# Performance work log

Measured on AMD Instinct MI355X. Metric: run time of the kernel, lower is better.

## Reference

```python
import jax, jax.numpy as jnp
import numpy as np

N_USERS, N_MOVIES = 200000, 80000
E, L = 2000000, 500000
D, H = 128, 64


def _mean_agg(x_src, src, dst, n_dst):
    # gather source features along edges and mean-reduce per destination node
    msg = x_src[src]                                        # [E, F]
    s = jax.ops.segment_sum(msg, dst, num_segments=n_dst)   # [n_dst, F]
    c = jax.ops.segment_sum(jnp.ones(src.shape, x_src.dtype), dst, num_segments=n_dst)
    return s / jnp.maximum(c, 1.0)[:, None]


def _sage(x_src, x_dst, src, dst, n_dst, Wl, b, Wr):
    # PyG SAGEConv (mean aggr): lin_l(mean_j x_j) + lin_r(x_dst); lin_r has no bias
    return _mean_agg(x_src, src, dst, n_dst) @ Wl + b + x_dst @ Wr


def setup_inputs() -> dict:
    key = jax.random.key(0)
    ks = jax.random.split(key, 24)
    inp = {
        "x_user": jax.random.normal(ks[0], (N_USERS, D), jnp.float32),
        "x_movie": jax.random.normal(ks[1], (N_MOVIES, D), jnp.float32),
        "edge_src": jax.random.randint(ks[2], (E,), 0, N_USERS, jnp.int32),
        "edge_dst": jax.random.randint(ks[3], (E,), 0, N_MOVIES, jnp.int32),
        "lbl_src": jax.random.randint(ks[4], (L,), 0, N_USERS, jnp.int32),
        "lbl_dst": jax.random.randint(ks[5], (L,), 0, N_MOVIES, jnp.int32),
    }
    def w(k, shape):
        fan_in = shape[0]
        return jax.random.uniform(k, shape, jnp.float32, -1.0, 1.0) / np.sqrt(fan_in)
    # layer 1 (src_dim D -> H), one SAGEConv per relation
    inp["W1_u2m_l"] = w(ks[6], (D, H)); inp["b1_u2m"] = jnp.zeros((H,), jnp.float32)
    inp["W1_u2m_r"] = w(ks[7], (D, H))
    inp["W1_m2u_l"] = w(ks[8], (D, H)); inp["b1_m2u"] = jnp.zeros((H,), jnp.float32)
    inp["W1_m2u_r"] = w(ks[9], (D, H))
    # layer 2 (H -> H)
    inp["W2_u2m_l"] = w(ks[10], (H, H)); inp["b2_u2m"] = jnp.zeros((H,), jnp.float32)
    inp["W2_u2m_r"] = w(ks[11], (H, H))
    inp["W2_m2u_l"] = w(ks[12], (H, H)); inp["b2_m2u"] = jnp.zeros((H,), jnp.float32)
    inp["W2_m2u_r"] = w(ks[13], (H, H))
    # edge decoder MLP
    inp["Wd1"] = w(ks[14], (2 * H, H)); inp["bd1"] = jnp.zeros((H,), jnp.float32)
    inp["Wd2"] = w(ks[15], (H, 1)); inp["bd2"] = jnp.zeros((1,), jnp.float32)
    return inp


def reference(x_user, x_movie, edge_src, edge_dst, lbl_src, lbl_dst,
              W1_u2m_l, b1_u2m, W1_u2m_r, W1_m2u_l, b1_m2u, W1_m2u_r,
              W2_u2m_l, b2_u2m, W2_u2m_r, W2_m2u_l, b2_m2u, W2_m2u_r,
              Wd1, bd1, Wd2, bd2):
    # hetero layer 1 (user->movie and movie->user reverse relation), then ReLU
    h_m = jax.nn.relu(_sage(x_user, x_movie, edge_src, edge_dst, N_MOVIES,
                            W1_u2m_l, b1_u2m, W1_u2m_r))
    h_u = jax.nn.relu(_sage(x_movie, x_user, edge_dst, edge_src, N_USERS,
                            W1_m2u_l, b1_m2u, W1_m2u_r))
    # hetero layer 2 (no activation, matching GNNEncoder)
    z_m = _sage(h_u, h_m, edge_src, edge_dst, N_MOVIES, W2_u2m_l, b2_u2m, W2_u2m_r)
    z_u = _sage(h_m, h_u, edge_dst, edge_src, N_USERS, W2_m2u_l, b2_m2u, W2_m2u_r)
    # edge decoder: gather-concat-MLP
    z = jnp.concatenate([z_u[lbl_src], z_m[lbl_dst]], axis=-1)  # [L, 2H]
    z = jax.nn.relu(z @ Wd1 + bd1)
    return (z @ Wd2 + bd2).reshape(-1)
```

## Files before the change

### kernel.cpp

```cpp
#include <hip/hip_runtime.h>
#include <stdint.h>

#define BW   128
#define NBM  625
#define NBU  1563
#define CAPM 4096
#define CAPU 2048

typedef __attribute__((ext_vector_type(8))) short bf16x8;
typedef __attribute__((ext_vector_type(4))) float f32x4;

__device__ __forceinline__ float b2f(ushort u) {
    return __uint_as_float((uint32_t)u << 16);
}
__device__ __forceinline__ ushort f2b(float f) {
    uint32_t x = __float_as_uint(f);
    return (ushort)((x + 0x7FFFu + ((x >> 16) & 1u)) >> 16);
}
__device__ __forceinline__ float lo16f(uint32_t v) { return __uint_as_float(v << 16); }
__device__ __forceinline__ float hi16f(uint32_t v) { return __uint_as_float(v & 0xFFFF0000u); }
__device__ __forceinline__ uint32_t packbf2(float x, float y) {
    return (uint32_t)f2b(x) | ((uint32_t)f2b(y) << 16);
}

__global__ __launch_bounds__(256) void bin_kernel(
    const int* __restrict__ src, const int* __restrict__ dst, int E,
    int* __restrict__ gcm, int* __restrict__ gcu,
    uint32_t* __restrict__ Bm, uint32_t* __restrict__ Bu)
{
    __shared__ int hm[NBM], hu[NBU];
    const int CH = 8192;
    int e0 = blockIdx.x * CH;
    int e1 = min(e0 + CH, E);
    int tid = threadIdx.x;
    for (int b = tid; b < NBM; b += 256) hm[b] = 0;
    for (int b = tid; b < NBU; b += 256) hu[b] = 0;
    __syncthreads();
    for (int i = e0 + tid; i < e1; i += 256) {
        atomicAdd(&hm[dst[i] >> 7], 1);
        atomicAdd(&hu[src[i] >> 7], 1);
    }
    __syncthreads();
    for (int b = tid; b < NBM; b += 256) { int c = hm[b]; hm[b] = c ? atomicAdd(&gcm[b], c) : 0; }
    for (int b = tid; b < NBU; b += 256) { int c = hu[b]; hu[b] = c ? atomicAdd(&gcu[b], c) : 0; }
    __syncthreads();
    for (int i = e0 + tid; i < e1; i += 256) {
        int d = dst[i], s = src[i];
        int bm = d >> 7, bu = s >> 7;
        int pm = atomicAdd(&hm[bm], 1);
        if (pm < CAPM) Bm[(size_t)bm * CAPM + pm] = ((uint32_t)(d & 127) << 24) | (uint32_t)s;
        int pu = atomicAdd(&hu[bu], 1);
        if (pu < CAPU) Bu[(size_t)bu * CAPU + pu] = ((uint32_t)(s & 127) << 24) | (uint32_t)d;
    }
}

__global__ __launch_bounds__(256) void sort_bucket2(
    uint32_t* __restrict__ Bm, const int* __restrict__ gcm, int* __restrict__ loffm,
    uint32_t* __restrict__ Bu, const int* __restrict__ gcu, int* __restrict__ loffu)
{
    __shared__ uint32_t rec[CAPM];
    __shared__ uint32_t srt[CAPM];
    __shared__ int hist[BW];
    __shared__ int hoff[BW + 1];
    __shared__ int cur[BW];
    int bid = blockIdx.x, tid = threadIdx.x;
    uint32_t* B; const int* gc; int* loff; int cap; int b;
    if (bid < NBM) { B = Bm; gc = gcm; loff = loffm; cap = CAPM; b = bid; }
    else           { B = Bu; gc = gcu; loff = loffu; cap = CAPU; b = bid - NBM; }
    int cnt = min(gc[b], cap);
    uint32_t* bp = B + (size_t)b * cap;
    for (int i = tid; i < cnt; i += 256) rec[i] = bp[i];
    if (tid < BW) hist[tid] = 0;
    __syncthreads();
    for (int i = tid; i < cnt; i += 256) atomicAdd(&hist[rec[i] >> 24], 1);
    __syncthreads();
    if (tid == 0) {
        int s = 0;
        for (int i = 0; i < BW; ++i) { hoff[i] = s; s += hist[i]; }
        hoff[BW] = s;
    }
    __syncthreads();
    if (tid < BW) cur[tid] = hoff[tid];
    __syncthreads();
    for (int i = tid; i < cnt; i += 256) {
        uint32_t r = rec[i];
        int pos = atomicAdd(&cur[r >> 24], 1);
        srt[pos] = (r & 0xFFFFFFu) << 5;
    }
    __syncthreads();
    for (int i = tid; i < cnt; i += 256) bp[i] = srt[i];
    for (int i = tid; i <= BW; i += 256) loff[(size_t)b * (BW + 1) + i] = hoff[i];
}

__global__ __launch_bounds__(256) void wprep(
    const float* __restrict__ W2ml, const float* __restrict__ W2mr,
    const float* __restrict__ W2ul, const float* __restrict__ W2ur,
    const float* __restrict__ Wd1, const float* __restrict__ bd1,
    const float* __restrict__ b2m, const float* __restrict__ b2u,
    const float* __restrict__ W1ul, const float* __restrict__ W1mr,
    const float* __restrict__ W1ml, const float* __restrict__ W1ur,
    ushort* __restrict__ Wt2_m, ushort* __restrict__ Wt2_u,
    ushort* __restrict__ Wt_u, ushort* __restrict__ Wt_m,
    float* __restrict__ cu, float* __restrict__ cm)
{
    __shared__ float As[4096], Bs[4096];
    int bid = blockIdx.x, tid = threadIdx.x;
    if (bid < 4) {
        const float* A; int brow0; const float* bvec; const float* addb;
        ushort* WtOut; int cofs; float* outc;
        if (bid == 0)      { A = W2ml; brow0 = 0;  bvec = b2m; addb = bd1;    WtOut = Wt2_m; cofs = 0;  outc = cu; }
        else if (bid == 1) { A = W2mr; brow0 = 0;  bvec = 0;   addb = 0;      WtOut = Wt2_u; cofs = 0;  outc = 0;  }
        else if (bid == 2) { A = W2ul; brow0 = 64; bvec = b2u; addb = 0;      WtOut = Wt2_u; cofs = 64; outc = cm; }
        else               { A = W2ur; brow0 = 64; bvec = 0;   addb = 0;      WtOut = Wt2_m; cofs = 64; outc = 0;  }
        for (int i = tid; i < 4096; i += 256) {
            As[i] = A[i];
            Bs[i] = Wd1[(size_t)(brow0 + (i >> 6)) * 64 + (i & 63)];
        }
        __syncthreads();
        int r = tid >> 2, c0 = (tid & 3) * 16;
        float acc[16] = {};
        for (int k = 0; k < 64; ++k) {
            float a = As[r * 64 + k];
            const float* bp = &Bs[k * 64 + c0];
#pragma unroll
            for (int j = 0; j < 16; ++j) acc[j] += a * bp[j];
        }
#pragma unroll
        for (int j = 0; j < 16; ++j)
            WtOut[(size_t)(cofs + c0 + j) * 64 + r] = f2b(acc[j]);
        if (outc && tid < 64) {
            float s = addb ? addb[tid] : 0.f;
            for (int k = 0; k < 64; ++k) s += bvec[k] * Bs[k * 64 + tid];
            outc[tid] = s;
        }
    } else {
        int t = bid - 4;
        const float *Wa, *Wb; ushort* Wt;
        if (t < 64) { Wa = W1ul; Wb = W1mr; Wt = Wt_u; }
        else        { Wa = W1ml; Wb = W1ur; Wt = Wt_m; t -= 64; }
        int idx = t * 256 + tid;
        int c = idx >> 7, k = idx & 127;
        Wt[idx] = f2b((c < 64 ? Wa : Wb)[(size_t)k * 64 + (c & 63)]);
    }
}

template<int RELU>
__global__ __launch_bounds__(256) void agg_csr(
    const uint32_t* __restrict__ Ba, const int* __restrict__ loffa, int capa,
    const uint32_t* __restrict__ ta, const uint32_t* __restrict__ sa,
    const float* __restrict__ biasa, uint32_t* __restrict__ oa, int na, int GA,
    const uint32_t* __restrict__ Bb, const int* __restrict__ loffb, int capb,
    const uint32_t* __restrict__ tb, const uint32_t* __restrict__ sb,
    const float* __restrict__ biasb, uint32_t* __restrict__ ob, int nb)
{
    int bid = blockIdx.x;
    const uint32_t* B; const int* loff; int cap;
    const uint32_t* table; const uint32_t* self; const float* bias;
    uint32_t* out; int n_nodes; int lb;
    if (bid < GA) { B = Ba; loff = loffa; cap = capa; table = ta; self = sa; bias = biasa; out = oa; n_nodes = na; lb = bid; }
    else          { B = Bb; loff = loffb; cap = capb; table = tb; self = sb; bias = biasb; out = ob; n_nodes = nb; lb = bid - GA; }
    int node = lb * 4 + (threadIdx.x >> 6);
    if (node >= n_nodes) return;
    int lane = threadIdx.x & 63;
    int eq = lane >> 4;
    int fq = lane & 15;
    int b = node >> 7, l = node & 127;
    const int* lo = loff + (size_t)b * (BW + 1);
    int beg = lo[l], end = lo[l + 1];
    const uint32_t* bp = B + (size_t)b * cap;
    float a0 = 0.f, a1 = 0.f, a2 = 0.f, a3 = 0.f;
    int p = beg;
    for (; p + 32 <= end; p += 32) {
        uint32_t r0 = bp[p + eq];
        uint32_t r1 = bp[p + 4 + eq];
        uint32_t r2 = bp[p + 8 + eq];
        uint32_t r3 = bp[p + 12 + eq];
        uint32_t r4 = bp[p + 16 + eq];
        uint32_t r5 = bp[p + 20 + eq];
        uint32_t r6 = bp[p + 24 + eq];
        uint32_t r7 = bp[p + 28 + eq];
        uint2 v0 = *(const uint2*)&table[r0 + fq * 2];
        uint2 v1 = *(const uint2*)&table[r1 + fq * 2];
        uint2 v2 = *(const uint2*)&table[r2 + fq * 2];
        uint2 v3 = *(const uint2*)&table[r3 + fq * 2];
        uint2 v4 = *(const uint2*)&table[r4 + fq * 2];
        uint2 v5 = *(const uint2*)&table[r5 + fq * 2];
        uint2 v6 = *(const uint2*)&table[r6 + fq * 2];
        uint2 v7 = *(const uint2*)&table[r7 + fq * 2];
        a0 += lo16f(v0.x) + lo16f(v1.x) + lo16f(v2.x) + lo16f(v3.x)
            + lo16f(v4.x) + lo16f(v5.x) + lo16f(v6.x) + lo16f(v7.x);
        a1 += hi16f(v0.x) + hi16f(v1.x) + hi16f(v2.x) + hi16f(v3.x)
            + hi16f(v4.x) + hi16f(v5.x) + hi16f(v6.x) + hi16f(v7.x);
        a2 += lo16f(v0.y) + lo16f(v1.y) + lo16f(v2.y) + lo16f(v3.y)
            + lo16f(v4.y) + lo16f(v5.y) + lo16f(v6.y) + lo16f(v7.y);
        a3 += hi16f(v0.y) + hi16f(v1.y) + hi16f(v2.y) + hi16f(v3.y)
            + hi16f(v4.y) + hi16f(v5.y) + hi16f(v6.y) + hi16f(v7.y);
    }
    for (; p + 8 <= end; p += 8) {
        uint32_t r0 = bp[p + eq];
        uint32_t r1 = bp[p + 4 + eq];
        uint2 v0 = *(const uint2*)&table[r0 + fq * 2];
        uint2 v1 = *(const uint2*)&table[r1 + fq * 2];
        a0 += lo16f(v0.x) + lo16f(v1.x);
        a1 += hi16f(v0.x) + hi16f(v1.x);
        a2 += lo16f(v0.y) + lo16f(v1.y);
        a3 += hi16f(v0.y) + hi16f(v1.y);
    }
    if (p + 4 <= end) {
        uint32_t r = bp[p + eq];
        uint2 v = *(const uint2*)&table[r + fq * 2];
        a0 += lo16f(v.x); a1 += hi16f(v.x); a2 += lo16f(v.y); a3 += hi16f(v.y);
        p += 4;
    }
    if (eq < end - p) {
        uint32_t r = bp[p + eq];
        uint2 v = *(const uint2*)&table[r + fq * 2];
        a0 += lo16f(v.x); a1 += hi16f(v.x); a2 += lo16f(v.y); a3 += hi16f(v.y);
    }
    a0 += __shfl_xor(a0, 16, 64); a0 += __shfl_xor(a0, 32, 64);
    a1 += __shfl_xor(a1, 16, 64); a1 += __shfl_xor(a1, 32, 64);
    a2 += __shfl_xor(a2, 16, 64); a2 += __shfl_xor(a2, 32, 64);
    a3 += __shfl_xor(a3, 16, 64); a3 += __shfl_xor(a3, 32, 64);
    if (lane < 16) {
        int deg = end - beg;
        float inv = 1.f / (float)(deg > 0 ? deg : 1);
        uint2 sv = *(const uint2*)&self[(size_t)node * 32 + fq * 2];
        float4 bv = *(const float4*)&bias[fq * 4];
        float v0 = a0 * inv + bv.x + lo16f(sv.x);
        float v1 = a1 * inv + bv.y + hi16f(sv.x);
        float v2 = a2 * inv + bv.z + lo16f(sv.y);
        float v3 = a3 * inv + bv.w + hi16f(sv.y);
        if (RELU) {
            v0 = fmaxf(v0, 0.f); v1 = fmaxf(v1, 0.f);
            v2 = fmaxf(v2, 0.f); v3 = fmaxf(v3, 0.f);
        }
        *(uint2*)&out[(size_t)node * 32 + fq * 2] = make_uint2(packbf2(v0, v1), packbf2(v2, v3));
    }
}

__global__ __launch_bounds__(256) void gemm1_mfma(
    const float* __restrict__ Xu, const ushort* __restrict__ Wtu,
    ushort* __restrict__ Ua, ushort* __restrict__ Ub, int Mu, int GU,
    const float* __restrict__ Xm, const ushort* __restrict__ Wtm,
    ushort* __restrict__ Ma, ushort* __restrict__ Mb, int Mm)
{
    constexpr int K = 128;
    int bid = blockIdx.x;
    const float* X; const ushort* Wt; ushort *Ya, *Yb; int row0; int M;
    if (bid < GU) { X = Xu; Wt = Wtu; Ya = Ua; Yb = Ub; row0 = bid * 128; M = Mu; }
    else          { X = Xm; Wt = Wtm; Ya = Ma; Yb = Mb; row0 = (bid - GU) * 128; M = Mm; }
    int tid = threadIdx.x;
    int lane = tid & 63, wr = tid >> 6;
    int r0g = row0 + wr * 32 + (lane & 15);
    int r1g = r0g + 16;
    int kgrp = (lane >> 4) * 8;
    f32x4 acc0[8] = {}, acc1[8] = {};
#pragma unroll
    for (int ks = 0; ks < 4; ++ks) {
        int kb = kgrp + ks * 32;
        float4 z = make_float4(0.f, 0.f, 0.f, 0.f);
        float4 u0 = z, u1 = z, w0 = z, w1 = z;
        if (r0g < M) {
            u0 = *(const float4*)&X[(size_t)r0g * K + kb];
            u1 = *(const float4*)&X[(size_t)r0g * K + kb + 4];
        }
        if (r1g < M) {
            w0 = *(const float4*)&X[(size_t)r1g * K + kb];
            w1 = *(const float4*)&X[(size_t)r1g * K + kb + 4];
        }
        float xs0[8] = {u0.x, u0.y, u0.z, u0.w, u1.x, u1.y, u1.z, u1.w};
        float xs1[8] = {w0.x, w0.y, w0.z, w0.w, w1.x, w1.y, w1.z, w1.w};
        bf16x8 ah0, al0, ah1, al1;
#pragma unroll
        for (int j = 0; j < 8; ++j) {
            ushort h0 = f2b(xs0[j]);
            ah0[j] = (short)h0;
            al0[j] = (short)f2b(xs0[j] - b2f(h0));
            ushort h1 = f2b(xs1[j]);
            ah1[j] = (short)h1;
            al1[j] = (short)f2b(xs1[j] - b2f(h1));
        }
#pragma unroll
        for (int cb = 0; cb < 8; ++cb) {
            bf16x8 b = *(const bf16x8*)&Wt[(size_t)(cb * 16 + (lane & 15)) * K + kb];
            acc0[cb] = __builtin_amdgcn_mfma_f32_16x16x32_bf16(ah0, b, acc0[cb], 0, 0, 0);
            acc0[cb] = __builtin_amdgcn_mfma_f32_16x16x32_bf16(al0, b, acc0[cb], 0, 0, 0);
            acc1[cb] = __builtin_amdgcn_mfma_f32_16x16x32_bf16(ah1, b, acc1[cb], 0, 0, 0);
            acc1[cb] = __builtin_amdgcn_mfma_f32_16x16x32_bf16(al1, b, acc1[cb], 0, 0, 0);
        }
    }
#pragma unroll
    for (int cb = 0; cb < 8; ++cb) {
        ushort* Y = (cb < 4) ? Ya : Yb;
        int cc = (cb * 16 + (lane & 15)) & 63;
#pragma unroll
        for (int reg = 0; reg < 4; ++reg) {
            int g0 = row0 + wr * 32 + (lane >> 4) * 4 + reg;
            if (g0 < M) Y[(size_t)g0 * 64 + cc] = f2b(acc0[cb][reg]);
            int g1 = g0 + 16;
            if (g1 < M) Y[(size_t)g1 * 64 + cc] = f2b(acc1[cb][reg]);
        }
    }
}

__global__ __launch_bounds__(256) void gemm2_mfma(
    const ushort* __restrict__ Xu, const ushort* __restrict__ Wtu,
    ushort* __restrict__ Ua, ushort* __restrict__ Ub, int Mu, int GU,
    const ushort* __restrict__ Xm, const ushort* __restrict__ Wtm,
    ushort* __restrict__ Ma, ushort* __restrict__ Mb, int Mm)
{
    int bid = blockIdx.x;
    const ushort* X; const ushort* Wt; ushort *Ya, *Yb; int row0;
    if (bid < GU) { X = Xu; Wt = Wtu; Ya = Ua; Yb = Ub; row0 = bid * 64; }
    else          { X = Xm; Wt = Wtm; Ya = Ma; Yb = Mb; row0 = (bid - GU) * 64; }
    int tid = threadIdx.x;
    int lane = tid & 63, wr = tid >> 6;
    int rglob = row0 + wr * 16 + (lane & 15);
    int kgrp = (lane >> 4) * 8;
    f32x4 acc[8] = {};
#pragma unroll
    for (int ks = 0; ks < 2; ++ks) {
        bf16x8 a = *(const bf16x8*)&X[(size_t)rglob * 64 + kgrp + ks * 32];
#pragma unroll
        for (int cb = 0; cb < 8; ++cb) {
            bf16x8 b = *(const bf16x8*)&Wt[(size_t)(cb * 16 + (lane & 15)) * 64 + kgrp + ks * 32];
            acc[cb] = __builtin_amdgcn_mfma_f32_16x16x32_bf16(a, b, acc[cb], 0, 0, 0);
        }
    }
#pragma unroll
    for (int cb = 0; cb < 8; ++cb) {
        ushort* Y = (cb < 4) ? Ya : Yb;
        int cc = (cb * 16 + (lane & 15)) & 63;
#pragma unroll
        for (int reg = 0; reg < 4; ++reg) {
            int grow = row0 + wr * 16 + (lane >> 4) * 4 + reg;
            Y[(size_t)grow * 64 + cc] = f2b(acc[cb][reg]);
        }
    }
}

__global__ __launch_bounds__(256) void edge_dec(
    const uint32_t* __restrict__ Au, const uint32_t* __restrict__ Am,
    const int* __restrict__ ls, const int* __restrict__ ld,
    const float* __restrict__ Wd2, const float* __restrict__ bd2,
    float* __restrict__ out, int L)
{
    int e0 = blockIdx.x * 32 + (threadIdx.x >> 4) * 2;
    if (e0 >= L) return;
    int e1 = e0 + 1;
    bool has1 = (e1 < L);
    int fq = threadIdx.x & 15;
    float4 w = *(const float4*)&Wd2[fq * 4];
    uint2 a0 = *(const uint2*)&Au[(size_t)ls[e0] * 32 + fq * 2];
    uint2 m0 = *(const uint2*)&Am[(size_t)ld[e0] * 32 + fq * 2];
    uint2 a1 = make_uint2(0u, 0u), m1 = make_uint2(0u, 0u);
    if (has1) {
        a1 = *(const uint2*)&Au[(size_t)ls[e1] * 32 + fq * 2];
        m1 = *(const uint2*)&Am[(size_t)ld[e1] * 32 + fq * 2];
    }
    float v0 = fmaxf(lo16f(a0.x) + lo16f(m0.x), 0.f) * w.x
             + fmaxf(hi16f(a0.x) + hi16f(m0.x), 0.f) * w.y
             + fmaxf(lo16f(a0.y) + lo16f(m0.y), 0.f) * w.z
             + fmaxf(hi16f(a0.y) + hi16f(m0.y), 0.f) * w.w;
    float v1 = fmaxf(lo16f(a1.x) + lo16f(m1.x), 0.f) * w.x
             + fmaxf(hi16f(a1.x) + hi16f(m1.x), 0.f) * w.y
             + fmaxf(lo16f(a1.y) + lo16f(m1.y), 0.f) * w.z
             + fmaxf(hi16f(a1.y) + hi16f(m1.y), 0.f) * w.w;
#pragma unroll
    for (int msk = 8; msk >= 1; msk >>= 1) {
        v0 += __shfl_xor(v0, msk, 64);
        v1 += __shfl_xor(v1, msk, 64);
    }
    if (fq == 0) {
        float b = bd2[0];
        out[e0] = v0 + b;
        if (has1) out[e1] = v1 + b;
    }
}

extern "C" void kernel_launch(void* const* d_in, const int* in_sizes, int n_in,
                              void* d_out, int out_size, void* d_ws, size_t ws_size,
                              hipStream_t stream)
{
    const float* x_user  = (const float*)d_in[0];
    const float* x_movie = (const float*)d_in[1];
    const int*   esrc    = (const int*)d_in[2];
    const int*   edst    = (const int*)d_in[3];
    const int*   lsrc    = (const int*)d_in[4];
    const int*   ldst    = (const int*)d_in[5];
    const float* W1ul = (const float*)d_in[6];
    const float* b1u  = (const float*)d_in[7];
    const float* W1ur = (const float*)d_in[8];
    const float* W1ml = (const float*)d_in[9];
    const float* b1m  = (const float*)d_in[10];
    const float* W1mr = (const float*)d_in[11];
    const float* W2ul = (const float*)d_in[12];
    const float* b2u  = (const float*)d_in[13];
    const float* W2ur = (const float*)d_in[14];
    const float* W2ml = (const float*)d_in[15];
    const float* b2m  = (const float*)d_in[16];
    const float* W2mr = (const float*)d_in[17];
    const float* Wd1  = (const float*)d_in[18];
    const float* bd1  = (const float*)d_in[19];
    const float* Wd2  = (const float*)d_in[20];
    const float* bd2  = (const float*)d_in[21];
    float* out = (float*)d_out;

    const int NU = in_sizes[0] / 128;
    const int NM = in_sizes[1] / 128;
    const int E  = in_sizes[2];
    const int L  = in_sizes[4];

    char* ws = (char*)d_ws;
    const size_t SU = (size_t)NU * 64 * 2;
    const size_t SM = (size_t)NM * 64 * 2;
    ushort* U0 = (ushort*)(ws + 0);
    ushort* U1 = (ushort*)(ws + SU);
    ushort* U2 = (ushort*)(ws + 2 * SU);
    ushort* M0 = (ushort*)(ws + 3 * SU);
    ushort* M1 = (ushort*)(ws + 3 * SU + SM);
    ushort* M2 = (ushort*)(ws + 3 * SU + 2 * SM);
    size_t o = 3 * SU + 3 * SM;
    auto align256 = [](size_t x) { return (x + 255) & ~(size_t)255; };
    o = align256(o);
    int* gcm = (int*)(ws + o); o = align256(o + (size_t)(NBM + NBU) * 4);
    int* gcu = gcm + NBM;
    uint32_t* Bm = (uint32_t*)(ws + o); o = align256(o + (size_t)NBM * CAPM * 4);
    uint32_t* Bu = (uint32_t*)(ws + o); o = align256(o + (size_t)NBU * CAPU * 4);
    int* loffm = (int*)(ws + o); o = align256(o + (size_t)NBM * (BW + 1) * 4);
    int* loffu = (int*)(ws + o); o = align256(o + (size_t)NBU * (BW + 1) * 4);
    float* cu  = (float*)(ws + o); o = align256(o + 64 * 4);
    float* cm  = (float*)(ws + o); o = align256(o + 64 * 4);
    ushort* Wt_u  = (ushort*)(ws + o); o = align256(o + 128 * 128 * 2);
    ushort* Wt_m  = (ushort*)(ws + o); o = align256(o + 128 * 128 * 2);
    ushort* Wt2_m = (ushort*)(ws + o); o = align256(o + 128 * 64 * 2);
    ushort* Wt2_u = (ushort*)(ws + o); o = align256(o + 128 * 64 * 2);

    hipMemsetAsync(gcm, 0, (size_t)(NBM + NBU) * 4, stream);
    int nbins = (E + 8191) / 8192;
    bin_kernel<<<nbins, 256, 0, stream>>>(esrc, edst, E, gcm, gcu, Bm, Bu);
    sort_bucket2<<<NBM + NBU, 256, 0, stream>>>(Bm, gcm, loffm, Bu, gcu, loffu);

    wprep<<<4 + 128, 256, 0, stream>>>(W2ml, W2mr, W2ul, W2ur, Wd1, bd1, b2m, b2u,
                                       W1ul, W1mr, W1ml, W1ur,
                                       Wt2_m, Wt2_u, Wt_u, Wt_m, cu, cm);

    int g1u = (NU + 127) / 128, g1m = (NM + 127) / 128;
    int gu = NU / 64, gm = NM / 64;
    int agm = (NM + 3) / 4, agu = (NU + 3) / 4;

    gemm1_mfma<<<g1u + g1m, 256, 0, stream>>>(x_user, Wt_u, U0, U1, NU, g1u,
                                              x_movie, Wt_m, M0, M1, NM);

    agg_csr<1><<<agm + agu, 256, 0, stream>>>(
        Bm, loffm, CAPM, (const uint32_t*)U0, (const uint32_t*)M1, b1u, (uint32_t*)M2, NM, agm,
        Bu, loffu, CAPU, (const uint32_t*)M0, (const uint32_t*)U1, b1m, (uint32_t*)U2, NU);

    gemm2_mfma<<<gu + gm, 256, 0, stream>>>(U2, Wt2_u, U0, U1, NU, gu,
                                            M2, Wt2_m, M0, M1, NM);

    agg_csr<0><<<agm + agu, 256, 0, stream>>>(
        Bm, loffm, CAPM, (const uint32_t*)U1, (const uint32_t*)M1, cm, (uint32_t*)M2, NM, agm,
        Bu, loffu, CAPU, (const uint32_t*)M0, (const uint32_t*)U0, cu, (uint32_t*)U2, NU);

    int gl = (L + 31) / 32;
    edge_dec<<<gl, 256, 0, stream>>>((const uint32_t*)U2, (const uint32_t*)M2,
                                     lsrc, ldst, Wd2, bd2, out, L);
}
```

Baseline: 464.8 us.

## Merge binning with weight prep and bucket sort with first GEMM

```diff
diff --git a/kernel.cpp b/kernel.cpp
--- a/kernel.cpp
+++ b/kernel.cpp
@@ -23,50 +23,168 @@
     return (uint32_t)f2b(x) | ((uint32_t)f2b(y) << 16);
 }
 
-__global__ __launch_bounds__(256) void bin_kernel(
-    const int* __restrict__ src, const int* __restrict__ dst, int E,
+__global__ __launch_bounds__(256) void binprep(
+    const int* __restrict__ src, const int* __restrict__ dst, int E, int nbins,
     int* __restrict__ gcm, int* __restrict__ gcu,
-    uint32_t* __restrict__ Bm, uint32_t* __restrict__ Bu)
-{
-    __shared__ int hm[NBM], hu[NBU];
-    const int CH = 8192;
-    int e0 = blockIdx.x * CH;
-    int e1 = min(e0 + CH, E);
-    int tid = threadIdx.x;
-    for (int b = tid; b < NBM; b += 256) hm[b] = 0;
-    for (int b = tid; b < NBU; b += 256) hu[b] = 0;
-    __syncthreads();
-    for (int i = e0 + tid; i < e1; i += 256) {
-        atomicAdd(&hm[dst[i] >> 7], 1);
-        atomicAdd(&hu[src[i] >> 7], 1);
-    }
-    __syncthreads();
-    for (int b = tid; b < NBM; b += 256) { int c = hm[b]; hm[b] = c ? atomicAdd(&gcm[b], c) : 0; }
-    for (int b = tid; b < NBU; b += 256) { int c = hu[b]; hu[b] = c ? atomicAdd(&gcu[b], c) : 0; }
-    __syncthreads();
-    for (int i = e0 + tid; i < e1; i += 256) {
-        int d = dst[i], s = src[i];
-        int bm = d >> 7, bu = s >> 7;
-        int pm = atomicAdd(&hm[bm], 1);
-        if (pm < CAPM) Bm[(size_t)bm * CAPM + pm] = ((uint32_t)(d & 127) << 24) | (uint32_t)s;
-        int pu = atomicAdd(&hu[bu], 1);
-        if (pu < CAPU) Bu[(size_t)bu * CAPU + pu] = ((uint32_t)(s & 127) << 24) | (uint32_t)d;
-    }
-}
-
-__global__ __launch_bounds__(256) void sort_bucket2(
+    uint32_t* __restrict__ Bm, uint32_t* __restrict__ Bu,
+    const float* __restrict__ W2ml, const float* __restrict__ W2mr,
+    const float* __restrict__ W2ul, const float* __restrict__ W2ur,
+    const float* __restrict__ Wd1, const float* __restrict__ bd1,
+    const float* __restrict__ b2m, const float* __restrict__ b2u,
+    const float* __restrict__ W1ul, const float* __restrict__ W1mr,
+    const float* __restrict__ W1ml, const float* __restrict__ W1ur,
+    ushort* __restrict__ Wt2_m, ushort* __restrict__ Wt2_u,
+    ushort* __restrict__ Wt_u, ushort* __restrict__ Wt_m,
+    float* __restrict__ cu, float* __restrict__ cm)
+{
+    __shared__ float smem[8192];
+    int bid = blockIdx.x, tid = threadIdx.x;
+    if (bid < nbins) {
+        int* hm = (int*)smem;
+        int* hu = ((int*)smem) + NBM;
+        const int CH = 8192;
+        int e0 = bid * CH;
+        int e1 = min(e0 + CH, E);
+        for (int b = tid; b < NBM; b += 256) hm[b] = 0;
+        for (int b = tid; b < NBU; b += 256) hu[b] = 0;
+        __syncthreads();
+        for (int i = e0 + tid; i < e1; i += 256) {
+            atomicAdd(&hm[dst[i] >> 7], 1);
+            atomicAdd(&hu[src[i] >> 7], 1);
+        }
+        __syncthreads();
+        for (int b = tid; b < NBM; b += 256) { int c = hm[b]; hm[b] = c ? atomicAdd(&gcm[b], c) : 0; }
+        for (int b = tid; b < NBU; b += 256) { int c = hu[b]; hu[b] = c ? atomicAdd(&gcu[b], c) : 0; }
+        __syncthreads();
+        for (int i = e0 + tid; i < e1; i += 256) {
+            int d = dst[i], s = src[i];
+            int bm = d >> 7, bu = s >> 7;
+            int pm = atomicAdd(&hm[bm], 1);
+            if (pm < CAPM) Bm[(size_t)bm * CAPM + pm] = ((uint32_t)(d & 127) << 24) | (uint32_t)s;
+            int pu = atomicAdd(&hu[bu], 1);
+            if (pu < CAPU) Bu[(size_t)bu * CAPU + pu] = ((uint32_t)(s & 127) << 24) | (uint32_t)d;
+        }
+        return;
+    }
+    int wb = bid - nbins;
+    if (wb < 4) {
+        float* As = smem;
+        float* Bs = smem + 4096;
+        const float* A; int brow0; const float* bvec; const float* addb;
+        ushort* WtOut; int cofs; float* outc;
+        if (wb == 0)      { A = W2ml; brow0 = 0;  bvec = b2m; addb = bd1;    WtOut = Wt2_m; cofs = 0;  outc = cu; }
+        else if (wb == 1) { A = W2mr; brow0 = 0;  bvec = 0;   addb = 0;      WtOut = Wt2_u; cofs = 0;  outc = 0;  }
+        else if (wb == 2) { A = W2ul; brow0 = 64; bvec = b2u; addb = 0;      WtOut = Wt2_u; cofs = 64; outc = cm; }
+        else              { A = W2ur; brow0 = 64; bvec = 0;   addb = 0;      WtOut = Wt2_m; cofs = 64; outc = 0;  }
+        for (int i = tid; i < 4096; i += 256) {
+            As[i] = A[i];
+            Bs[i] = Wd1[(size_t)(brow0 + (i >> 6)) * 64 + (i & 63)];
+        }
+        __syncthreads();
+        int r = tid >> 2, c0 = (tid & 3) * 16;
+        float acc[16] = {};
+        for (int k = 0; k < 64; ++k) {
+            float a = As[r * 64 + k];
+            const float* bp = &Bs[k * 64 + c0];
+#pragma unroll
+            for (int j = 0; j < 16; ++j) acc[j] += a * bp[j];
+        }
+#pragma unroll
+        for (int j = 0; j < 16; ++j)
+            WtOut[(size_t)(cofs + c0 + j) * 64 + r] = f2b(acc[j]);
+        if (outc && tid < 64) {
+            float s = addb ? addb[tid] : 0.f;
+            for (int k = 0; k < 64; ++k) s += bvec[k] * Bs[k * 64 + tid];
+            outc[tid] = s;
+        }
+    } else {
+        int t = wb - 4;
+        const float *Wa, *Wb; ushort* Wt;
+        if (t < 64) { Wa = W1ul; Wb = W1mr; Wt = Wt_u; }
+        else        { Wa = W1ml; Wb = W1ur; Wt = Wt_m; t -= 64; }
+        int idx = t * 256 + tid;
+        int c = idx >> 7, k = idx & 127;
+        Wt[idx] = f2b((c < 64 ? Wa : Wb)[(size_t)k * 64 + (c & 63)]);
+    }
+}
+
+__global__ __launch_bounds__(256) void sortgemm1(
+    const float* __restrict__ Xu, const ushort* __restrict__ Wtu,
+    ushort* __restrict__ Ua, ushort* __restrict__ Ub, int Mu, int GU,
+    const float* __restrict__ Xm, const ushort* __restrict__ Wtm,
+    ushort* __restrict__ Ma, ushort* __restrict__ Mb, int Mm, int NG,
     uint32_t* __restrict__ Bm, const int* __restrict__ gcm, int* __restrict__ loffm,
     uint32_t* __restrict__ Bu, const int* __restrict__ gcu, int* __restrict__ loffu)
 {
-    __shared__ uint32_t rec[CAPM];
-    __shared__ uint32_t srt[CAPM];
-    __shared__ int hist[BW];
-    __shared__ int hoff[BW + 1];
-    __shared__ int cur[BW];
+    __shared__ uint32_t smem[2 * CAPM + 3 * BW + 1];
     int bid = blockIdx.x, tid = threadIdx.x;
+    if (bid < NG) {
+        constexpr int K = 128;
+        const float* X; const ushort* Wt; ushort *Ya, *Yb; int row0; int M;
+        if (bid < GU) { X = Xu; Wt = Wtu; Ya = Ua; Yb = Ub; row0 = bid * 128; M = Mu; }
+        else          { X = Xm; Wt = Wtm; Ya = Ma; Yb = Mb; row0 = (bid - GU) * 128; M = Mm; }
+        int lane = tid & 63, wr = tid >> 6;
+        int r0g = row0 + wr * 32 + (lane & 15);
+        int r1g = r0g + 16;
+        int kgrp = (lane >> 4) * 8;
+        f32x4 acc0[8] = {}, acc1[8] = {};
+#pragma unroll
+        for (int ks = 0; ks < 4; ++ks) {
+            int kb = kgrp + ks * 32;
+            float4 z = make_float4(0.f, 0.f, 0.f, 0.f);
+            float4 u0 = z, u1 = z, w0 = z, w1 = z;
+            if (r0g < M) {
+                u0 = *(const float4*)&X[(size_t)r0g * K + kb];
+                u1 = *(const float4*)&X[(size_t)r0g * K + kb + 4];
+            }
+            if (r1g < M) {
+                w0 = *(const float4*)&X[(size_t)r1g * K + kb];
+                w1 = *(const float4*)&X[(size_t)r1g * K + kb + 4];
+            }
+            float xs0[8] = {u0.x, u0.y, u0.z, u0.w, u1.x, u1.y, u1.z, u1.w};
+            float xs1[8] = {w0.x, w0.y, w0.z, w0.w, w1.x, w1.y, w1.z, w1.w};
+            bf16x8 ah0, al0, ah1, al1;
+#pragma unroll
+            for (int j = 0; j < 8; ++j) {
+                ushort h0 = f2b(xs0[j]);
+                ah0[j] = (short)h0;
+                al0[j] = (short)f2b(xs0[j] - b2f(h0));
+                ushort h1 = f2b(xs1[j]);
+                ah1[j] = (short)h1;
+                al1[j] = (short)f2b(xs1[j] - b2f(h1));
+            }
+#pragma unroll
+            for (int cb = 0; cb < 8; ++cb) {
+                bf16x8 b = *(const bf16x8*)&Wt[(size_t)(cb * 16 + (lane & 15)) * K + kb];
+                acc0[cb] = __builtin_amdgcn_mfma_f32_16x16x32_bf16(ah0, b, acc0[cb], 0, 0, 0);
+                acc0[cb] = __builtin_amdgcn_mfma_f32_16x16x32_bf16(al0, b, acc0[cb], 0, 0, 0);
+                acc1[cb] = __builtin_amdgcn_mfma_f32_16x16x32_bf16(ah1, b, acc1[cb], 0, 0, 0);
+                acc1[cb] = __builtin_amdgcn_mfma_f32_16x16x32_bf16(al1, b, acc1[cb], 0, 0, 0);
+            }
+        }
+#pragma unroll
+        for (int cb = 0; cb < 8; ++cb) {
+            ushort* Y = (cb < 4) ? Ya : Yb;
+            int cc = (cb * 16 + (lane & 15)) & 63;
+#pragma unroll
+            for (int reg = 0; reg < 4; ++reg) {
+                int g0 = row0 + wr * 32 + (lane >> 4) * 4 + reg;
+                if (g0 < M) Y[(size_t)g0 * 64 + cc] = f2b(acc0[cb][reg]);
+                int g1 = g0 + 16;
+                if (g1 < M) Y[(size_t)g1 * 64 + cc] = f2b(acc1[cb][reg]);
+            }
+        }
+        return;
+    }
+    int sbid = bid - NG;
+    uint32_t* rec = smem;
+    uint32_t* srt = smem + CAPM;
+    int* hist = (int*)(smem + 2 * CAPM);
+    int* hoff = hist + BW;
+    int* cur  = hoff + BW + 1;
     uint32_t* B; const int* gc; int* loff; int cap; int b;
-    if (bid < NBM) { B = Bm; gc = gcm; loff = loffm; cap = CAPM; b = bid; }
-    else           { B = Bu; gc = gcu; loff = loffu; cap = CAPU; b = bid - NBM; }
+    if (sbid < NBM) { B = Bm; gc = gcm; loff = loffm; cap = CAPM; b = sbid; }
+    else            { B = Bu; gc = gcu; loff = loffu; cap = CAPU; b = sbid - NBM; }
     int cnt = min(gc[b], cap);
     uint32_t* bp = B + (size_t)b * cap;
     for (int i = tid; i < cnt; i += 256) rec[i] = bp[i];
@@ -90,58 +208,6 @@
     __syncthreads();
     for (int i = tid; i < cnt; i += 256) bp[i] = srt[i];
     for (int i = tid; i <= BW; i += 256) loff[(size_t)b * (BW + 1) + i] = hoff[i];
-}
-
-__global__ __launch_bounds__(256) void wprep(
-    const float* __restrict__ W2ml, const float* __restrict__ W2mr,
-    const float* __restrict__ W2ul, const float* __restrict__ W2ur,
-    const float* __restrict__ Wd1, const float* __restrict__ bd1,
-    const float* __restrict__ b2m, const float* __restrict__ b2u,
-    const float* __restrict__ W1ul, const float* __restrict__ W1mr,
-    const float* __restrict__ W1ml, const float* __restrict__ W1ur,
-    ushort* __restrict__ Wt2_m, ushort* __restrict__ Wt2_u,
-    ushort* __restrict__ Wt_u, ushort* __restrict__ Wt_m,
-    float* __restrict__ cu, float* __restrict__ cm)
-{
-    __shared__ float As[4096], Bs[4096];
-    int bid = blockIdx.x, tid = threadIdx.x;
-    if (bid < 4) {
-        const float* A; int brow0; const float* bvec; const float* addb;
-        ushort* WtOut; int cofs; float* outc;
-        if (bid == 0)      { A = W2ml; brow0 = 0;  bvec = b2m; addb = bd1;    WtOut = Wt2_m; cofs = 0;  outc = cu; }
-        else if (bid == 1) { A = W2mr; brow0 = 0;  bvec = 0;   addb = 0;      WtOut = Wt2_u; cofs = 0;  outc = 0;  }
-        else if (bid == 2) { A = W2ul; brow0 = 64; bvec = b2u; addb = 0;      WtOut = Wt2_u; cofs = 64; outc = cm; }
-        else               { A = W2ur; brow0 = 64; bvec = 0;   addb = 0;      WtOut = Wt2_m; cofs = 64; outc = 0;  }
-        for (int i = tid; i < 4096; i += 256) {
-            As[i] = A[i];
-            Bs[i] = Wd1[(size_t)(brow0 + (i >> 6)) * 64 + (i & 63)];
-        }
-        __syncthreads();
-        int r = tid >> 2, c0 = (tid & 3) * 16;
-        float acc[16] = {};
-        for (int k = 0; k < 64; ++k) {
-            float a = As[r * 64 + k];
-            const float* bp = &Bs[k * 64 + c0];
-#pragma unroll
-            for (int j = 0; j < 16; ++j) acc[j] += a * bp[j];
-        }
-#pragma unroll
-        for (int j = 0; j < 16; ++j)
-            WtOut[(size_t)(cofs + c0 + j) * 64 + r] = f2b(acc[j]);
-        if (outc && tid < 64) {
-            float s = addb ? addb[tid] : 0.f;
-            for (int k = 0; k < 64; ++k) s += bvec[k] * Bs[k * 64 + tid];
-            outc[tid] = s;
-        }
-    } else {
-        int t = bid - 4;
-        const float *Wa, *Wb; ushort* Wt;
-        if (t < 64) { Wa = W1ul; Wb = W1mr; Wt = Wt_u; }
-        else        { Wa = W1ml; Wb = W1ur; Wt = Wt_m; t -= 64; }
-        int idx = t * 256 + tid;
-        int c = idx >> 7, k = idx & 127;
-        Wt[idx] = f2b((c < 64 ? Wa : Wb)[(size_t)k * 64 + (c & 63)]);
-    }
 }
 
 template<int RELU>
@@ -170,31 +236,19 @@
     const uint32_t* bp = B + (size_t)b * cap;
     float a0 = 0.f, a1 = 0.f, a2 = 0.f, a3 = 0.f;
     int p = beg;
-    for (; p + 32 <= end; p += 32) {
+    for (; p + 16 <= end; p += 16) {
         uint32_t r0 = bp[p + eq];
         uint32_t r1 = bp[p + 4 + eq];
         uint32_t r2 = bp[p + 8 + eq];
         uint32_t r3 = bp[p + 12 + eq];
-        uint32_t r4 = bp[p + 16 + eq];
-        uint32_t r5 = bp[p + 20 + eq];
-        uint32_t r6 = bp[p + 24 + eq];
-        uint32_t r7 = bp[p + 28 + eq];
         uint2 v0 = *(const uint2*)&table[r0 + fq * 2];
         uint2 v1 = *(const uint2*)&table[r1 + fq * 2];
         uint2 v2 = *(const uint2*)&table[r2 + fq * 2];
         uint2 v3 = *(const uint2*)&table[r3 + fq * 2];
-        uint2 v4 = *(const uint2*)&table[r4 + fq * 2];
-        uint2 v5 = *(const uint2*)&table[r5 + fq * 2];
-        uint2 v6 = *(const uint2*)&table[r6 + fq * 2];
-        uint2 v7 = *(const uint2*)&table[r7 + fq * 2];
-        a0 += lo16f(v0.x) + lo16f(v1.x) + lo16f(v2.x) + lo16f(v3.x)
-            + lo16f(v4.x) + lo16f(v5.x) + lo16f(v6.x) + lo16f(v7.x);
-        a1 += hi16f(v0.x) + hi16f(v1.x) + hi16f(v2.x) + hi16f(v3.x)
-            + hi16f(v4.x) + hi16f(v5.x) + hi16f(v6.x) + hi16f(v7.x);
-        a2 += lo16f(v0.y) + lo16f(v1.y) + lo16f(v2.y) + lo16f(v3.y)
-            + lo16f(v4.y) + lo16f(v5.y) + lo16f(v6.y) + lo16f(v7.y);
-        a3 += hi16f(v0.y) + hi16f(v1.y) + hi16f(v2.y) + hi16f(v3.y)
-            + hi16f(v4.y) + hi16f(v5.y) + hi16f(v6.y) + hi16f(v7.y);
+        a0 += lo16f(v0.x) + lo16f(v1.x) + lo16f(v2.x) + lo16f(v3.x);
+        a1 += hi16f(v0.x) + hi16f(v1.x) + hi16f(v2.x) + hi16f(v3.x);
+        a2 += lo16f(v0.y) + lo16f(v1.y) + lo16f(v2.y) + lo16f(v3.y);
+        a3 += hi16f(v0.y) + hi16f(v1.y) + hi16f(v2.y) + hi16f(v3.y);
     }
     for (; p + 8 <= end; p += 8) {
         uint32_t r0 = bp[p + eq];
@@ -235,71 +289,6 @@
             v2 = fmaxf(v2, 0.f); v3 = fmaxf(v3, 0.f);
         }
         *(uint2*)&out[(size_t)node * 32 + fq * 2] = make_uint2(packbf2(v0, v1), packbf2(v2, v3));
-    }
-}
-
-__global__ __launch_bounds__(256) void gemm1_mfma(
-    const float* __restrict__ Xu, const ushort* __restrict__ Wtu,
-    ushort* __restrict__ Ua, ushort* __restrict__ Ub, int Mu, int GU,
-    const float* __restrict__ Xm, const ushort* __restrict__ Wtm,
-    ushort* __restrict__ Ma, ushort* __restrict__ Mb, int Mm)
-{
-    constexpr int K = 128;
-    int bid = blockIdx.x;
-    const float* X; const ushort* Wt; ushort *Ya, *Yb; int row0; int M;
-    if (bid < GU) { X = Xu; Wt = Wtu; Ya = Ua; Yb = Ub; row0 = bid * 128; M = Mu; }
-    else          { X = Xm; Wt = Wtm; Ya = Ma; Yb = Mb; row0 = (bid - GU) * 128; M = Mm; }
-    int tid = threadIdx.x;
-    int lane = tid & 63, wr = tid >> 6;
-    int r0g = row0 + wr * 32 + (lane & 15);
-    int r1g = r0g + 16;
-    int kgrp = (lane >> 4) * 8;
-    f32x4 acc0[8] = {}, acc1[8] = {};
-#pragma unroll
-    for (int ks = 0; ks < 4; ++ks) {
-        int kb = kgrp + ks * 32;
-        float4 z = make_float4(0.f, 0.f, 0.f, 0.f);
-        float4 u0 = z, u1 = z, w0 = z, w1 = z;
-        if (r0g < M) {
-            u0 = *(const float4*)&X[(size_t)r0g * K + kb];
-            u1 = *(const float4*)&X[(size_t)r0g * K + kb + 4];
-        }
-        if (r1g < M) {
-            w0 = *(const float4*)&X[(size_t)r1g * K + kb];
-            w1 = *(const float4*)&X[(size_t)r1g * K + kb + 4];
-        }
-        float xs0[8] = {u0.x, u0.y, u0.z, u0.w, u1.x, u1.y, u1.z, u1.w};
-        float xs1[8] = {w0.x, w0.y, w0.z, w0.w, w1.x, w1.y, w1.z, w1.w};
-        bf16x8 ah0, al0, ah1, al1;
-#pragma unroll
-        for (int j = 0; j < 8; ++j) {
-            ushort h0 = f2b(xs0[j]);
-            ah0[j] = (short)h0;
-            al0[j] = (short)f2b(xs0[j] - b2f(h0));
-            ushort h1 = f2b(xs1[j]);
-            ah1[j] = (short)h1;
-            al1[j] = (short)f2b(xs1[j] - b2f(h1));
-        }
-#pragma unroll
-        for (int cb = 0; cb < 8; ++cb) {
-            bf16x8 b = *(const bf16x8*)&Wt[(size_t)(cb * 16 + (lane & 15)) * K + kb];
-            acc0[cb] = __builtin_amdgcn_mfma_f32_16x16x32_bf16(ah0, b, acc0[cb], 0, 0, 0);
-            acc0[cb] = __builtin_amdgcn_mfma_f32_16x16x32_bf16(al0, b, acc0[cb], 0, 0, 0);
-            acc1[cb] = __builtin_amdgcn_mfma_f32_16x16x32_bf16(ah1, b, acc1[cb], 0, 0, 0);
-            acc1[cb] = __builtin_amdgcn_mfma_f32_16x16x32_bf16(al1, b, acc1[cb], 0, 0, 0);
-        }
-    }
-#pragma unroll
-    for (int cb = 0; cb < 8; ++cb) {
-        ushort* Y = (cb < 4) ? Ya : Yb;
-        int cc = (cb * 16 + (lane & 15)) & 63;
-#pragma unroll
-        for (int reg = 0; reg < 4; ++reg) {
-            int g0 = row0 + wr * 32 + (lane >> 4) * 4 + reg;
-            if (g0 < M) Y[(size_t)g0 * 64 + cc] = f2b(acc0[cb][reg]);
-            int g1 = g0 + 16;
-            if (g1 < M) Y[(size_t)g1 * 64 + cc] = f2b(acc1[cb][reg]);
-        }
     }
 }
 
@@ -436,21 +425,21 @@
     ushort* Wt2_m = (ushort*)(ws + o); o = align256(o + 128 * 64 * 2);
     ushort* Wt2_u = (ushort*)(ws + o); o = align256(o + 128 * 64 * 2);
 
-    hipMemsetAsync(gcm, 0, (size_t)(NBM + NBU) * 4, stream);
-    int nbins = (E + 8191) / 8192;
-    bin_kernel<<<nbins, 256, 0, stream>>>(esrc, edst, E, gcm, gcu, Bm, Bu);
-    sort_bucket2<<<NBM + NBU, 256, 0, stream>>>(Bm, gcm, loffm, Bu, gcu, loffu);
-
-    wprep<<<4 + 128, 256, 0, stream>>>(W2ml, W2mr, W2ul, W2ur, Wd1, bd1, b2m, b2u,
-                                       W1ul, W1mr, W1ml, W1ur,
-                                       Wt2_m, Wt2_u, Wt_u, Wt_m, cu, cm);
-
     int g1u = (NU + 127) / 128, g1m = (NM + 127) / 128;
     int gu = NU / 64, gm = NM / 64;
     int agm = (NM + 3) / 4, agu = (NU + 3) / 4;
-
-    gemm1_mfma<<<g1u + g1m, 256, 0, stream>>>(x_user, Wt_u, U0, U1, NU, g1u,
-                                              x_movie, Wt_m, M0, M1, NM);
+    int nbins = (E + 8191) / 8192;
+
+    hipMemsetAsync(gcm, 0, (size_t)(NBM + NBU) * 4, stream);
+    binprep<<<nbins + 132, 256, 0, stream>>>(esrc, edst, E, nbins, gcm, gcu, Bm, Bu,
+                                             W2ml, W2mr, W2ul, W2ur, Wd1, bd1, b2m, b2u,
+                                             W1ul, W1mr, W1ml, W1ur,
+                                             Wt2_m, Wt2_u, Wt_u, Wt_m, cu, cm);
+
+    sortgemm1<<<(g1u + g1m) + (NBM + NBU), 256, 0, stream>>>(
+        x_user, Wt_u, U0, U1, NU, g1u,
+        x_movie, Wt_m, M0, M1, NM, g1u + g1m,
+        Bm, gcm, loffm, Bu, gcu, loffu);
 
     agg_csr<1><<<agm + agu, 256, 0, stream>>>(
         Bm, loffm, CAPM, (const uint32_t*)U0, (const uint32_t*)M1, b1u, (uint32_t*)M2, NM, agm,
```

After: 446.2 us, median of 2. 4.0% less time.
